# Performance work log

Measured on AMD Instinct MI355X. Metric: run time of the kernel, lower is better.

Reference implementation:

```python
import jax, jax.numpy as jnp
import numpy as np

N_QUBITS = 10
Q_DEPTH = 6


def _apply_1q(state, gate, wire):
    """Apply a 2x2 gate (or batched [B,2,2] gates) to `wire` of state [B,2,...,2]."""
    s = jnp.moveaxis(state, wire + 1, -1)
    if gate.ndim == 2:
        s = s @ gate.T  # new_j = sum_i G[j,i] * old_i
    else:
        s = jnp.einsum('b...i,bji->b...j', s, gate)
    return jnp.moveaxis(s, -1, wire + 1)


def _apply_cnot(state, ctrl, tgt):
    s = jnp.moveaxis(state, (ctrl + 1, tgt + 1), (-2, -1))
    s = jnp.stack([s[..., 0, :], s[..., 1, ::-1]], axis=-2)  # flip target where ctrl=1
    return jnp.moveaxis(s, (-2, -1), (ctrl + 1, tgt + 1))


def _ry(theta):
    """RY(theta) = [[cos(t/2), -sin(t/2)], [sin(t/2), cos(t/2)]]; theta scalar or [B]."""
    c, s = jnp.cos(theta / 2.0), jnp.sin(theta / 2.0)
    return jnp.stack([jnp.stack([c, -s], -1), jnp.stack([s, c], -1)], -2)


def _vqc(angles, q_weights):
    """angles: [B, n_qubits] per-sample RY angles; q_weights: [q_depth, n_qubits].
    Returns <PauliZ_w> for every wire: [B, n_qubits]. All gates are real -> float32 state."""
    B, n = angles.shape
    q_depth = q_weights.shape[0]
    # H-layer on |0...0> gives the uniform superposition: all amplitudes 2^{-n/2}
    state = jnp.full((B,) + (2,) * n, 2.0 ** (-n / 2.0), dtype=angles.dtype)
    # RY layer with per-sample input angles
    for w in range(n):
        state = _apply_1q(state, _ry(angles[:, w]), w)
    # q_depth x (brick-wall CNOT entangler + trainable RY layer)
    for k in range(q_depth):
        for i in range(0, n - 1, 2):
            state = _apply_cnot(state, i, i + 1)
        for i in range(1, n - 1, 2):
            state = _apply_cnot(state, i, i + 1)
        for w in range(n):
            state = _apply_1q(state, _ry(q_weights[k, w]), w)
    # expval(PauliZ(w)) = P(wire w = 0) - P(wire w = 1)
    probs = state * state  # real statevector
    exps = []
    for w in range(n):
        p = jnp.moveaxis(probs, w + 1, 1).reshape(B, 2, -1).sum(-1)
        exps.append(p[:, 0] - p[:, 1])
    return jnp.stack(exps, -1)


def setup_inputs() -> dict:
    key = jax.random.key(0)
    ks = jax.random.split(key, 6)
    B, D_IN, OUT = 8192, 512, 64
    x = jax.random.normal(ks[0], (B, D_IN), dtype=jnp.float32)
    W1 = jax.random.normal(ks[1], (D_IN, N_QUBITS), dtype=jnp.float32) * (1.0 / np.sqrt(D_IN))
    b1 = jnp.zeros((N_QUBITS,), dtype=jnp.float32)
    # keras 'uniform' initializer: U(-0.05, 0.05)
    q_weights = jax.random.uniform(ks[2], (Q_DEPTH, N_QUBITS), dtype=jnp.float32,
                                   minval=-0.05, maxval=0.05)
    W2 = jax.random.normal(ks[3], (N_QUBITS, OUT), dtype=jnp.float32) * (1.0 / np.sqrt(N_QUBITS))
    b2 = jnp.zeros((OUT,), dtype=jnp.float32)
    return {"x": x, "W1": W1, "b1": b1, "q_weights": q_weights, "W2": W2, "b2": b2}


def reference(x, W1, b1, q_weights, W2, b2):
    # Dense(n_qubits, tanh) then scale to angles in (-pi/2, pi/2)
    angles = jnp.tanh(x @ W1 + b1) * (jnp.pi / 2.0)  # [B, n_qubits]
    q_out = _vqc(angles, q_weights)                   # [B, n_qubits]
    return q_out @ W2 + b2                            # [B, output_dim]
```

## Files before the change

### kernel.cpp

```cpp
#include <hip/hip_runtime.h>

#define NQ 10
#define QD 6
#define DIN 512
#define DOUT 64

template <int CTRL>
__device__ __forceinline__ float dppf(float v) {
    return __int_as_float(__builtin_amdgcn_mov_dpp(__float_as_int(v), CTRL, 0xF, 0xF, true));
}
template <int M>
__device__ __forceinline__ float sx(float v) {
    if constexpr (M == 1)       return dppf<0xB1>(v);
    else if constexpr (M == 2)  return dppf<0x4E>(v);
    else if constexpr (M == 4)  return dppf<0x1B>(dppf<0x141>(v));
    else                        return dppf<0x128>(v);
}
__device__ __forceinline__ float swz16(float v) {
    return __int_as_float(__builtin_amdgcn_ds_swizzle(__float_as_int(v), 0x401F));
}
__device__ __forceinline__ float sx32(float v, int xaddr) {
    return __int_as_float(__builtin_amdgcn_ds_bpermute(xaddr, __float_as_int(v)));
}
__device__ __forceinline__ float red64(float v, int xaddr) {
    v += dppf<0x128>(v);
    v += dppf<0x124>(v);
    v += dppf<0x122>(v);
    v += dppf<0x121>(v);
    v += swz16(v);
    v += sx32(v, xaddr);
    return v;
}
__device__ __forceinline__ float tanh_fast(float x) {
    const float e = __expf(2.0f * x);
    return 1.0f - __fdividef(2.0f, e + 1.0f);
}

__global__ __launch_bounds__(256) void dqc_main(
    const float* __restrict__ x,
    const float* __restrict__ W1,
    const float* __restrict__ b1,
    const float* __restrict__ qw,
    const float* __restrict__ W2,
    const float* __restrict__ b2,
    float* __restrict__ out,
    const int B)
{
    __shared__ __align__(16) float csl[QD * 24];

    const int tid = threadIdx.x;
    if (tid < QD * NQ) {
        const int layer = tid / NQ, wire = tid - layer * NQ;
        const float h = qw[tid] * 0.5f;
        const int pos = layer * 24 + (wire & 1) * 12 + (wire >> 1) * 2;
        csl[pos] = __cosf(h); csl[pos + 1] = __sinf(h);
    }

    const int lane = tid & 63;
    const int b = blockIdx.x * 4 + (tid >> 6);
    const int bb = (b < B) ? b : (B - 1);
    const int xaddr = ((tid ^ 32) & 63) << 2;

    float xr[8];
    {
        const float4* xp = (const float4*)(x + (size_t)bb * DIN + lane * 8);
        const float4 v0 = xp[0], v1 = xp[1];
        xr[0]=v0.x; xr[1]=v0.y; xr[2]=v0.z; xr[3]=v0.w;
        xr[4]=v1.x; xr[5]=v1.y; xr[6]=v1.z; xr[7]=v1.w;
    }
    float dot[NQ];
    #pragma unroll
    for (int w = 0; w < NQ; ++w) dot[w] = 0.f;
    {
        const float4* wp = (const float4*)(W1 + (size_t)lane * 8 * NQ);
        #pragma unroll
        for (int j = 0; j < 4; ++j) {
            const float4 f0 = wp[5*j], f1 = wp[5*j+1], f2 = wp[5*j+2],
                         f3 = wp[5*j+3], f4 = wp[5*j+4];
            const float xa = xr[2*j], xb = xr[2*j+1];
            dot[0]=fmaf(xa,f0.x,dot[0]); dot[1]=fmaf(xa,f0.y,dot[1]);
            dot[2]=fmaf(xa,f0.z,dot[2]); dot[3]=fmaf(xa,f0.w,dot[3]);
            dot[4]=fmaf(xa,f1.x,dot[4]); dot[5]=fmaf(xa,f1.y,dot[5]);
            dot[6]=fmaf(xa,f1.z,dot[6]); dot[7]=fmaf(xa,f1.w,dot[7]);
            dot[8]=fmaf(xa,f2.x,dot[8]); dot[9]=fmaf(xa,f2.y,dot[9]);
            dot[0]=fmaf(xb,f2.z,dot[0]); dot[1]=fmaf(xb,f2.w,dot[1]);
            dot[2]=fmaf(xb,f3.x,dot[2]); dot[3]=fmaf(xb,f3.y,dot[3]);
            dot[4]=fmaf(xb,f3.z,dot[4]); dot[5]=fmaf(xb,f3.w,dot[5]);
            dot[6]=fmaf(xb,f4.x,dot[6]); dot[7]=fmaf(xb,f4.y,dot[7]);
            dot[8]=fmaf(xb,f4.z,dot[8]); dot[9]=fmaf(xb,f4.w,dot[9]);
        }
    }
    #pragma unroll
    for (int w = 0; w < NQ; ++w) dot[w] = red64(dot[w], xaddr);

    float u0[NQ], u1[NQ];
    #pragma unroll
    for (int w = 0; w < NQ; ++w) {
        const float phi = fmaf(tanh_fast(dot[w] + b1[w]),
                               0.78539816339744830962f, 0.78539816339744830962f);
        u0[w] = __cosf(phi);
        u1[w] = __sinf(phi);
    }

    float A[16];
    {
        float lf = ((lane & 32) ? u1[0] : u0[0]);
        lf *= ((((lane >> 4) ^ (lane >> 5)) & 1) ? u1[1] : u0[1]);
        lf *= ((lane & 8) ? u1[2] : u0[2]);
        lf *= ((((lane >> 2) ^ (lane >> 3)) & 1) ? u1[3] : u0[3]);
        lf *= ((lane & 2) ? u1[4] : u0[4]);
        lf *= (((lane ^ (lane >> 1)) & 1) ? u1[5] : u0[5]);
        #pragma unroll
        for (int r = 0; r < 16; ++r) {
            float f = ((r & 8) ? u1[6] : u0[6]);
            f *= ((((r >> 2) ^ (r >> 3)) & 1) ? u1[7] : u0[7]);
            f *= ((r & 2) ? u1[8] : u0[8]);
            f *= ((((r >> 1) ^ r) & 1) ? u1[9] : u0[9]);
            A[r] = f * lf;
        }
    }

    __syncthreads();

    #pragma unroll 1
    for (int k = 0; k < QD; ++k) {
        const float* ce = csl + k * 24;
        const bool fuse = (k != QD - 1);

        const float4 ea = *(const float4*)(ce);
        const float4 eb = *(const float4*)(ce + 4);
        const float2 ec = *(const float2*)(ce + 8);
        const float C0=ea.x,S0=ea.y, C2=ea.z,S2=ea.w;
        const float C4=eb.x,S4=eb.y, C6=eb.z,S6=eb.w;
        const float C8=ec.x,S8=ec.y;

        {
            const float g = (lane & 32) ? S0 : -S0;
            float p[16];
            #pragma unroll
            for (int r = 0; r < 16; ++r) p[r] = sx32(A[r], xaddr);
            #pragma unroll
            for (int r = 0; r < 16; ++r) A[r] = fmaf(C0, A[r], g * p[r]);
        }
        {
            const float g = (lane & 8) ? S2 : -S2;
            const bool cb = (lane & 16) != 0;
            const float al = cb ? g : C2, be = cb ? C2 : g;
            #pragma unroll
            for (int r = 0; r < 16; ++r) A[r] = fmaf(al, A[r], be * sx<8>(A[r]));
        }
        {
            const float g = (lane & 2) ? S4 : -S4;
            const bool cb = (lane & 4) != 0;
            const float al = cb ? g : C4, be = cb ? C4 : g;
            #pragma unroll
            for (int r = 0; r < 16; ++r) A[r] = fmaf(al, A[r], be * sx<2>(A[r]));
        }
        {
            const bool cb = (lane & 1) != 0;
            const float a_lo = cb ? -S6 : C6, b_lo = cb ? C6 : -S6;
            const float a_hi = cb ?  S6 : C6, b_hi = cb ? C6 :  S6;
            #pragma unroll
            for (int r = 0; r < 8; ++r) {
                const float lo = A[r], hi = A[r + 8];
                A[r]     = fmaf(a_lo, lo, b_lo * hi);
                A[r + 8] = fmaf(a_hi, hi, b_hi * lo);
            }
        }
        {
            #pragma unroll
            for (int r = 0; r < 16; ++r) {
                if (r & 2) continue;
                const float lo = A[r], hi = A[r + 2];
                if (r & 4) {
                    A[r]     = fmaf(-S8, lo, C8 * hi);
                    A[r + 2] = fmaf( S8, hi, C8 * lo);
                } else {
                    A[r]     = fmaf(C8, lo, -S8 * hi);
                    A[r + 2] = fmaf(C8, hi,  S8 * lo);
                }
            }
        }

        const float4 oa = *(const float4*)(ce + 12);
        const float4 ob = *(const float4*)(ce + 16);
        const float2 oc = *(const float2*)(ce + 20);
        const float C1=oa.x,S1=oa.y, C3=oa.z,S3=oa.w;
        const float C5=ob.x,S5=ob.y, C7=ob.z,S7=ob.w;
        const float C9=oc.x,S9=oc.y;

        {
            const float g = (lane & 16) ? S1 : -S1;
            const bool cb = fuse && ((lane & 32) != 0);
            const float al = cb ? -g : C1, be = cb ? C1 : g;
            float p[16];
            #pragma unroll
            for (int r = 0; r < 16; ++r) p[r] = swz16(A[r]);
            #pragma unroll
            for (int r = 0; r < 16; ++r) A[r] = fmaf(al, A[r], be * p[r]);
        }
        {
            const float g = (lane & 4) ? S3 : -S3;
            const bool cb = fuse && ((lane & 8) != 0);
            const float al = cb ? -g : C3, be = cb ? C3 : g;
            #pragma unroll
            for (int r = 0; r < 16; ++r) A[r] = fmaf(al, A[r], be * sx<4>(A[r]));
        }
        {
            const float g = (lane & 1) ? S5 : -S5;
            const bool cb = fuse && ((lane & 2) != 0);
            const float al = cb ? -g : C5, be = cb ? C5 : g;
            #pragma unroll
            for (int r = 0; r < 16; ++r) A[r] = fmaf(al, A[r], be * sx<1>(A[r]));
        }
        {
            #pragma unroll
            for (int r = 0; r < 16; ++r) {
                if (r & 4) continue;
                const float lo = A[r], hi = A[r + 4];
                if (fuse && (r & 8)) {
                    A[r]     = fmaf( S7, lo, C7 * hi);
                    A[r + 4] = fmaf(-S7, hi, C7 * lo);
                } else {
                    A[r]     = fmaf(C7, lo, -S7 * hi);
                    A[r + 4] = fmaf(C7, hi,  S7 * lo);
                }
            }
        }
        {
            #pragma unroll
            for (int r = 0; r < 16; r += 2) {
                const float xv = A[r], yv = A[r + 1];
                if (fuse && (r & 2)) {
                    A[r]     = fmaf( S9, xv, C9 * yv);
                    A[r + 1] = fmaf(-S9, yv, C9 * xv);
                } else {
                    A[r]     = fmaf(C9, xv, -S9 * yv);
                    A[r + 1] = fmaf(C9, yv,  S9 * xv);
                }
            }
        }
    }

    float tot = 0.f, q6 = 0.f, q7 = 0.f, q8 = 0.f, q9 = 0.f;
    #pragma unroll
    for (int r = 0; r < 16; ++r) {
        const float P = A[r] * A[r];
        tot += P;
        if (r & 8) q6 += P;
        if (r & 4) q7 += P;
        if (r & 2) q8 += P;
        if (r & 1) q9 += P;
    }
    float e[NQ];
    e[0] = (lane & 32) ? -tot : tot;
    e[1] = (lane & 16) ? -tot : tot;
    e[2] = (lane & 8)  ? -tot : tot;
    e[3] = (lane & 4)  ? -tot : tot;
    e[4] = (lane & 2)  ? -tot : tot;
    e[5] = (lane & 1)  ? -tot : tot;
    e[6] = fmaf(-2.f, q6, tot);
    e[7] = fmaf(-2.f, q7, tot);
    e[8] = fmaf(-2.f, q8, tot);
    e[9] = fmaf(-2.f, q9, tot);
    #pragma unroll
    for (int w = 0; w < NQ; ++w) e[w] = red64(e[w], xaddr);

    if (b < B) {
        float o = b2[lane];
        #pragma unroll
        for (int w = 0; w < NQ; ++w) o = fmaf(e[w], W2[w * DOUT + lane], o);
        out[(size_t)b * DOUT + lane] = o;
    }
}

extern "C" void kernel_launch(void* const* d_in, const int* in_sizes, int n_in,
                              void* d_out, int out_size, void* d_ws, size_t ws_size,
                              hipStream_t stream) {
    const float* x  = (const float*)d_in[0];
    const float* W1 = (const float*)d_in[1];
    const float* b1 = (const float*)d_in[2];
    const float* qw = (const float*)d_in[3];
    const float* W2 = (const float*)d_in[4];
    const float* b2 = (const float*)d_in[5];
    float* out = (float*)d_out;

    const int B = in_sizes[0] / DIN;
    const int blocks = (B + 3) / 4;
    dqc_main<<<blocks, 256, 0, stream>>>(x, W1, b1, qw, W2, b2, out, B);
}
```

Measured before the change: 107.2 us.

## Factor cosines out of RY rotations into a global scale, using tangents

Rewrites several RY rotations (wires 0,7,8,9 in every layer, plus wires 1,3,5 in the last layer) in tangent form, so each output element needs one FMA instead of a multiply plus an FMA. The product of the factored-out cosines is folded into the initial state amplitude. The initial product-state build is also restructured as a shared prefix tree. The cost is per-block tangent precomputation, an extra syncthreads earlier in the kernel, and accuracy risk if a cosine were near zero, which these small weights avoid.

```diff
diff --git a/kernel.cpp b/kernel.cpp
--- a/kernel.cpp
+++ b/kernel.cpp
@@ -23,10 +23,8 @@
     return __int_as_float(__builtin_amdgcn_ds_bpermute(xaddr, __float_as_int(v)));
 }
 __device__ __forceinline__ float red64(float v, int xaddr) {
-    v += dppf<0x128>(v);
-    v += dppf<0x124>(v);
-    v += dppf<0x122>(v);
-    v += dppf<0x121>(v);
+    v += dppf<0x128>(v); v += dppf<0x124>(v);
+    v += dppf<0x122>(v); v += dppf<0x121>(v);
     v += swz16(v);
     v += sx32(v, xaddr);
     return v;
@@ -47,13 +45,21 @@
     const int B)
 {
     __shared__ __align__(16) float csl[QD * 24];
+    __shared__ __align__(16) float tsl[QD * 8];
 
     const int tid = threadIdx.x;
     if (tid < QD * NQ) {
         const int layer = tid / NQ, wire = tid - layer * NQ;
         const float h = qw[tid] * 0.5f;
+        const float s = __sinf(h), c = __cosf(h);
         const int pos = layer * 24 + (wire & 1) * 12 + (wire >> 1) * 2;
-        csl[pos] = __cosf(h); csl[pos + 1] = __sinf(h);
+        csl[pos] = c; csl[pos + 1] = s;
+        int slot = -1;
+        if (wire == 0) slot = 0; else if (wire == 7) slot = 1;
+        else if (wire == 8) slot = 2; else if (wire == 9) slot = 3;
+        else if (wire == 1) slot = 4; else if (wire == 3) slot = 5;
+        else if (wire == 5) slot = 6;
+        if (slot >= 0) tsl[layer * 8 + slot] = __fdividef(s, c);
     }
 
     const int lane = tid & 63;
@@ -102,6 +108,20 @@
         u1[w] = __sinf(phi);
     }
 
+    __syncthreads();
+
+    float F = 1.f;
+    #pragma unroll
+    for (int k = 0; k < QD; ++k) {
+        const float* ce = csl + k * 24;
+        F *= ce[0] * ce[18];
+        F *= ce[8] * ce[20];
+    }
+    {   const float* c5 = csl + 5 * 24;
+        F *= c5[12] * c5[14];
+        F *= c5[16];
+    }
+
     float A[16];
     {
         float lf = ((lane & 32) ? u1[0] : u0[0]);
@@ -110,37 +130,41 @@
         lf *= ((((lane >> 2) ^ (lane >> 3)) & 1) ? u1[3] : u0[3]);
         lf *= ((lane & 2) ? u1[4] : u0[4]);
         lf *= (((lane ^ (lane >> 1)) & 1) ? u1[5] : u0[5]);
-        #pragma unroll
-        for (int r = 0; r < 16; ++r) {
-            float f = ((r & 8) ? u1[6] : u0[6]);
-            f *= ((((r >> 2) ^ (r >> 3)) & 1) ? u1[7] : u0[7]);
-            f *= ((r & 2) ? u1[8] : u0[8]);
-            f *= ((((r >> 1) ^ r) & 1) ? u1[9] : u0[9]);
-            A[r] = f * lf;
-        }
-    }
-
-    __syncthreads();
+        lf *= F;
+        float d1[2] = { lf * u0[6], lf * u1[6] };
+        float d2[4], d3[8];
+        #pragma unroll
+        for (int i = 0; i < 4; ++i) {
+            const int r3 = i >> 1, r2 = i & 1;
+            d2[i] = d1[r3] * (((r2 ^ r3) & 1) ? u1[7] : u0[7]);
+        }
+        #pragma unroll
+        for (int i = 0; i < 8; ++i)
+            d3[i] = d2[i >> 1] * ((i & 1) ? u1[8] : u0[8]);
+        #pragma unroll
+        for (int i = 0; i < 8; ++i) {
+            const int r1 = i & 1;
+            A[2*i]   = d3[i] * (r1 ? u1[9] : u0[9]);
+            A[2*i+1] = d3[i] * (r1 ? u0[9] : u1[9]);
+        }
+    }
 
     #pragma unroll 1
     for (int k = 0; k < QD; ++k) {
         const float* ce = csl + k * 24;
-        const bool fuse = (k != QD - 1);
-
         const float4 ea = *(const float4*)(ce);
         const float4 eb = *(const float4*)(ce + 4);
-        const float2 ec = *(const float2*)(ce + 8);
-        const float C0=ea.x,S0=ea.y, C2=ea.z,S2=ea.w;
-        const float C4=eb.x,S4=eb.y, C6=eb.z,S6=eb.w;
-        const float C8=ec.x,S8=ec.y;
-
-        {
-            const float g = (lane & 32) ? S0 : -S0;
+        const float4 tv = *(const float4*)(tsl + k * 8);
+        const float C2=ea.z,S2=ea.w, C4=eb.x,S4=eb.y, C6=eb.z,S6=eb.w;
+        const float T0=tv.x, T7=tv.y, T8=tv.z, T9=tv.w;
+
+        {
+            const float t0 = (lane & 32) ? T0 : -T0;
             float p[16];
             #pragma unroll
             for (int r = 0; r < 16; ++r) p[r] = sx32(A[r], xaddr);
             #pragma unroll
-            for (int r = 0; r < 16; ++r) A[r] = fmaf(C0, A[r], g * p[r]);
+            for (int r = 0; r < 16; ++r) A[r] = fmaf(t0, p[r], A[r]);
         }
         {
             const float g = (lane & 8) ? S2 : -S2;
@@ -173,70 +197,108 @@
                 if (r & 2) continue;
                 const float lo = A[r], hi = A[r + 2];
                 if (r & 4) {
-                    A[r]     = fmaf(-S8, lo, C8 * hi);
-                    A[r + 2] = fmaf( S8, hi, C8 * lo);
+                    A[r]     = fmaf(-T8, lo, hi);
+                    A[r + 2] = fmaf( T8, hi, lo);
                 } else {
-                    A[r]     = fmaf(C8, lo, -S8 * hi);
-                    A[r + 2] = fmaf(C8, hi,  S8 * lo);
-                }
-            }
-        }
-
-        const float4 oa = *(const float4*)(ce + 12);
-        const float4 ob = *(const float4*)(ce + 16);
-        const float2 oc = *(const float2*)(ce + 20);
-        const float C1=oa.x,S1=oa.y, C3=oa.z,S3=oa.w;
-        const float C5=ob.x,S5=ob.y, C7=ob.z,S7=ob.w;
-        const float C9=oc.x,S9=oc.y;
-
-        {
-            const float g = (lane & 16) ? S1 : -S1;
-            const bool cb = fuse && ((lane & 32) != 0);
-            const float al = cb ? -g : C1, be = cb ? C1 : g;
-            float p[16];
-            #pragma unroll
-            for (int r = 0; r < 16; ++r) p[r] = swz16(A[r]);
-            #pragma unroll
-            for (int r = 0; r < 16; ++r) A[r] = fmaf(al, A[r], be * p[r]);
-        }
-        {
-            const float g = (lane & 4) ? S3 : -S3;
-            const bool cb = fuse && ((lane & 8) != 0);
-            const float al = cb ? -g : C3, be = cb ? C3 : g;
-            #pragma unroll
-            for (int r = 0; r < 16; ++r) A[r] = fmaf(al, A[r], be * sx<4>(A[r]));
-        }
-        {
-            const float g = (lane & 1) ? S5 : -S5;
-            const bool cb = fuse && ((lane & 2) != 0);
-            const float al = cb ? -g : C5, be = cb ? C5 : g;
-            #pragma unroll
-            for (int r = 0; r < 16; ++r) A[r] = fmaf(al, A[r], be * sx<1>(A[r]));
-        }
-        {
-            #pragma unroll
-            for (int r = 0; r < 16; ++r) {
-                if (r & 4) continue;
-                const float lo = A[r], hi = A[r + 4];
-                if (fuse && (r & 8)) {
-                    A[r]     = fmaf( S7, lo, C7 * hi);
-                    A[r + 4] = fmaf(-S7, hi, C7 * lo);
-                } else {
-                    A[r]     = fmaf(C7, lo, -S7 * hi);
-                    A[r + 4] = fmaf(C7, hi,  S7 * lo);
-                }
-            }
-        }
-        {
-            #pragma unroll
-            for (int r = 0; r < 16; r += 2) {
-                const float xv = A[r], yv = A[r + 1];
-                if (fuse && (r & 2)) {
-                    A[r]     = fmaf( S9, xv, C9 * yv);
-                    A[r + 1] = fmaf(-S9, yv, C9 * xv);
-                } else {
-                    A[r]     = fmaf(C9, xv, -S9 * yv);
-                    A[r + 1] = fmaf(C9, yv,  S9 * xv);
+                    A[r]     = fmaf(-T8, hi, lo);
+                    A[r + 2] = fmaf( T8, lo, hi);
+                }
+            }
+        }
+
+        if (k != QD - 1) {
+            const float4 oa = *(const float4*)(ce + 12);
+            const float2 ob = *(const float2*)(ce + 16);
+            const float C1=oa.x,S1=oa.y, C3=oa.z,S3=oa.w, C5=ob.x,S5=ob.y;
+
+            {
+                const float g = (lane & 16) ? S1 : -S1;
+                const bool cb = (lane & 32) != 0;
+                const float al = cb ? -g : C1, be = cb ? C1 : g;
+                float p[16];
+                #pragma unroll
+                for (int r = 0; r < 16; ++r) p[r] = swz16(A[r]);
+                #pragma unroll
+                for (int r = 0; r < 16; ++r) A[r] = fmaf(al, A[r], be * p[r]);
+            }
+            {
+                const float g = (lane & 4) ? S3 : -S3;
+                const bool cb = (lane & 8) != 0;
+                const float al = cb ? -g : C3, be = cb ? C3 : g;
+                #pragma unroll
+                for (int r = 0; r < 16; ++r) A[r] = fmaf(al, A[r], be * sx<4>(A[r]));
+            }
+            {
+                const float g = (lane & 1) ? S5 : -S5;
+                const bool cb = (lane & 2) != 0;
+                const float al = cb ? -g : C5, be = cb ? C5 : g;
+                #pragma unroll
+                for (int r = 0; r < 16; ++r) A[r] = fmaf(al, A[r], be * sx<1>(A[r]));
+            }
+            {
+                #pragma unroll
+                for (int r = 0; r < 16; ++r) {
+                    if (r & 4) continue;
+                    const float lo = A[r], hi = A[r + 4];
+                    if (r & 8) {
+                        A[r]     = fmaf( T7, lo, hi);
+                        A[r + 4] = fmaf(-T7, hi, lo);
+                    } else {
+                        A[r]     = fmaf(-T7, hi, lo);
+                        A[r + 4] = fmaf( T7, lo, hi);
+                    }
+                }
+            }
+            {
+                #pragma unroll
+                for (int r = 0; r < 16; r += 2) {
+                    const float xv = A[r], yv = A[r + 1];
+                    if (r & 2) {
+                        A[r]     = fmaf( T9, xv, yv);
+                        A[r + 1] = fmaf(-T9, yv, xv);
+                    } else {
+                        A[r]     = fmaf(-T9, yv, xv);
+                        A[r + 1] = fmaf( T9, xv, yv);
+                    }
+                }
+            }
+        } else {
+            const float4 tv2 = *(const float4*)(tsl + k * 8 + 4);
+            const float T1 = tv2.x, T3 = tv2.y, T5 = tv2.z;
+
+            {
+                const float t1 = (lane & 16) ? T1 : -T1;
+                float p[16];
+                #pragma unroll
+                for (int r = 0; r < 16; ++r) p[r] = swz16(A[r]);
+                #pragma unroll
+                for (int r = 0; r < 16; ++r) A[r] = fmaf(t1, p[r], A[r]);
+            }
+            {
+                const float t3 = (lane & 4) ? T3 : -T3;
+                #pragma unroll
+                for (int r = 0; r < 16; ++r) A[r] = fmaf(t3, sx<4>(A[r]), A[r]);
+            }
+            {
+                const float t5 = (lane & 1) ? T5 : -T5;
+                #pragma unroll
+                for (int r = 0; r < 16; ++r) A[r] = fmaf(t5, sx<1>(A[r]), A[r]);
+            }
+            {
+                #pragma unroll
+                for (int r = 0; r < 16; ++r) {
+                    if (r & 4) continue;
+                    const float lo = A[r], hi = A[r + 4];
+                    A[r]     = fmaf(-T7, hi, lo);
+                    A[r + 4] = fmaf( T7, lo, hi);
+                }
+            }
+            {
+                #pragma unroll
+                for (int r = 0; r < 16; r += 2) {
+                    const float xv = A[r], yv = A[r + 1];
+                    A[r]     = fmaf(-T9, yv, xv);
+                    A[r + 1] = fmaf( T9, xv, yv);
                 }
             }
         }
```

New measurement: 100.6 us (median of 2 runs). -6.2%, faster.
